# Performance work log

Measured on AMD Instinct MI355X. Metric: run time of the kernel, lower is better.

Reference implementation:

```python
import jax, jax.numpy as jnp
import numpy as np

EMBED = 1024
HEADS = 16
HEAD_DIM = EMBED // HEADS
B, S = 2, 2048


def setup_inputs() -> dict:
    key = jax.random.key(0)
    ks = jax.random.split(key, 9)
    std = 1.0 / np.sqrt(EMBED)
    def lin(k):
        kw, kb = jax.random.split(k)
        W = jax.random.uniform(kw, (EMBED, EMBED), jnp.float32, -std, std)
        b = jax.random.uniform(kb, (EMBED,), jnp.float32, -std, std)
        return W, b
    Wq, bq = lin(ks[0])
    Wk, bk = lin(ks[1])
    Wv, bv = lin(ks[2])
    Wo, bo = lin(ks[3])
    x = jax.random.normal(ks[4], (B, S, EMBED), jnp.float32)
    return {"x": x, "Wq": Wq, "bq": bq, "Wk": Wk, "bk": bk,
            "Wv": Wv, "bv": bv, "Wo": Wo, "bo": bo}


def reference(x, Wq, bq, Wk, bk, Wv, bv, Wo, bo):
    b, s, e = x.shape
    # projections (torch Linear: x @ W^T + b; here W stored as [in,out])
    Q = x @ Wq + bq
    K = x @ Wk + bk
    V = x @ Wv + bv
    # [b, h, s, d]
    Q = Q.reshape(b, s, HEADS, HEAD_DIM).transpose(0, 2, 1, 3)
    K = K.reshape(b, s, HEADS, HEAD_DIM).transpose(0, 2, 1, 3)
    V = V.reshape(b, s, HEADS, HEAD_DIM).transpose(0, 2, 1, 3)
    scores = jnp.einsum('bhqd,bhkd->bhqk', Q, K) / np.sqrt(HEAD_DIM)
    # causal mask: positions k > q masked to -inf
    causal = jnp.tril(jnp.ones((s, s), dtype=bool))
    scores = jnp.where(causal[None, None], scores, -jnp.inf)
    weights = jax.nn.softmax(scores, axis=-1)
    out = jnp.einsum('bhqk,bhkd->bhqd', weights, V)
    out = out.transpose(0, 2, 1, 3).reshape(b, s, e)
    return out @ Wo + bo
```

## Files before the change

### kernel.cpp

```cpp
#include <hip/hip_runtime.h>
#include <hip/hip_bf16.h>
#include <stdint.h>

#define EMBED 1024
#define HEADS 16
#define HDIM 64
#define BATCH 2
#define SEQ 2048
#define NROWS (BATCH*SEQ)

typedef __attribute__((ext_vector_type(8))) short short8;
typedef __attribute__((ext_vector_type(4))) float f32x4;

#define LOG2E 1.44269504088896f

__device__ __forceinline__ unsigned short f2bf(float f) {
    __hip_bfloat16 b = __float2bfloat16(f);
    return *reinterpret_cast<unsigned short*>(&b);
}

__device__ __forceinline__ unsigned cvt_pk_bf16(float lo, float hi) {
    unsigned r;
    asm("v_cvt_pk_bf16_f32 %0, %1, %2" : "=v"(r) : "v"(lo), "v"(hi));
    return r;
}

__device__ __forceinline__ short8 mk8(unsigned a, unsigned b, unsigned c, unsigned d) {
    union { unsigned u[4]; short8 s; } x;
    x.u[0] = a; x.u[1] = b; x.u[2] = c; x.u[3] = d;
    return x.s;
}

__device__ __forceinline__ void g2l16(const void* g, void* l) {
    __builtin_amdgcn_global_load_lds(
        (const __attribute__((address_space(1))) unsigned int*)g,
        (__attribute__((address_space(3))) unsigned int*)l, 16, 0, 0);
}

__global__ void prep_kernel(const float* __restrict__ x,
                            unsigned short* __restrict__ xb,
                            const float* __restrict__ W0,
                            const float* __restrict__ W1,
                            const float* __restrict__ W2,
                            const float* __restrict__ W3,
                            unsigned short* __restrict__ dst) {
    __shared__ float tile[32][33];
    const int id = blockIdx.x;
    const int t = threadIdx.x;
    if (id < 4096) {
        const int z = id >> 10;
        const int by = (id >> 5) & 31;
        const int bx = id & 31;
        const float* W = (z == 0) ? W0 : (z == 1) ? W1 : (z == 2) ? W2 : W3;
        unsigned short* Wt = dst + (size_t)z * EMBED * EMBED;
        const int tx = t & 31, ty = t >> 5;
#pragma unroll
        for (int r = 0; r < 4; r++) {
            int i = by * 32 + ty + r * 8;
            int o = bx * 32 + tx;
            tile[ty + r * 8][tx] = W[(size_t)i * EMBED + o];
        }
        __syncthreads();
        int i2 = by * 32 + tx;
#pragma unroll
        for (int r = 0; r < 4; r++) {
            int o2 = bx * 32 + ty + r * 8;
            Wt[(size_t)o2 * EMBED + i2] = f2bf(tile[tx][ty + r * 8]);
        }
    } else {
        int i = (id - 4096) * 256 + t;
        float4 v = reinterpret_cast<const float4*>(x)[i];
        ushort4 o;
        o.x = f2bf(v.x); o.y = f2bf(v.y); o.z = f2bf(v.z); o.w = f2bf(v.w);
        reinterpret_cast<ushort4*>(xb)[i] = o;
    }
}

template<int MODE, int BM, int BN, int PIPE>
__global__ __launch_bounds__(256)
void gemm_kernel(const unsigned short* __restrict__ A,
                 const unsigned short* __restrict__ B,
                 int K,
                 unsigned short* __restrict__ Qo,
                 unsigned short* __restrict__ Ko,
                 unsigned short* __restrict__ Vto,
                 const float* __restrict__ bq,
                 const float* __restrict__ bk,
                 const float* __restrict__ bvv,
                 float* __restrict__ Co,
                 const float* __restrict__ bo) {
    constexpr int AI = BM / 32;
    constexpr int BJ = BN / 32;
    constexpr int NBUF = PIPE ? 2 : 1;
    __shared__ __attribute__((aligned(16))) unsigned short As[NBUF][BM * 64];
    __shared__ __attribute__((aligned(16))) unsigned short Bs[NBUF][BN * 64];
    const int t = threadIdx.x;
    const int lane = t & 63;
    const int w = t >> 6;
    const int wr = w >> 1, wc = w & 1;
    const int l15 = lane & 15, l16 = lane >> 4;

    int bx, by;
    {
        const int xcd = blockIdx.x & 7;
        const int r = blockIdx.x >> 3;
        if (MODE == 0) {
            bx = (xcd & 1) * 12 + r % 12;
            by = (xcd >> 1) * 8 + r / 12;
        } else {
            bx = r & 15;
            by = xcd * 8 + (r >> 4);
        }
    }
    const int m0 = by * BM;
    const int n0 = bx * BN;

    f32x4 acc[AI][BJ];
#pragma unroll
    for (int i = 0; i < AI; i++)
#pragma unroll
        for (int j = 0; j < BJ; j++) acc[i][j] = (f32x4){0.f, 0.f, 0.f, 0.f};

    auto stage = [&](int k0, int buf) {
#pragma unroll
        for (int i = 0; i < BM / 32; i++) {
            int c = i * 256 + t;
            int row = c >> 3;
            int lc = (c & 7) ^ (row & 7);
            g2l16(A + (size_t)(m0 + row) * K + k0 + lc * 8,
                  As[buf] + (size_t)(i * 256 + (t & ~63)) * 8);
        }
#pragma unroll
        for (int i = 0; i < BN / 32; i++) {
            int c = i * 256 + t;
            int row = c >> 3;
            int lc = (c & 7) ^ (row & 7);
            g2l16(B + (size_t)(n0 + row) * K + k0 + lc * 8,
                  Bs[buf] + (size_t)(i * 256 + (t & ~63)) * 8);
        }
    };

    auto compute = [&](int buf) {
#pragma unroll
        for (int kk = 0; kk < 2; kk++) {
            short8 a[AI], b[BJ];
#pragma unroll
            for (int ai = 0; ai < AI; ai++) {
                int row = wr * (BM / 2) + ai * 16 + l15;
                int ch = kk * 4 + l16;
                a[ai] = *reinterpret_cast<const short8*>(
                    As[buf] + row * 64 + ((ch ^ (row & 7)) << 3));
            }
#pragma unroll
            for (int bj = 0; bj < BJ; bj++) {
                int row = wc * (BN / 2) + bj * 16 + l15;
                int ch = kk * 4 + l16;
                b[bj] = *reinterpret_cast<const short8*>(
                    Bs[buf] + row * 64 + ((ch ^ (row & 7)) << 3));
            }
            __builtin_amdgcn_s_setprio(1);
#pragma unroll
            for (int ai = 0; ai < AI; ai++)
#pragma unroll
                for (int bj = 0; bj < BJ; bj++)
                    acc[ai][bj] = __builtin_amdgcn_mfma_f32_16x16x32_bf16(
                        a[ai], b[bj], acc[ai][bj], 0, 0, 0);
            __builtin_amdgcn_s_setprio(0);
        }
    };

    if (PIPE) {
        const int ntk = K >> 6;
        stage(0, 0);
        asm volatile("s_waitcnt vmcnt(0)" ::: "memory");
        __builtin_amdgcn_s_barrier();
        asm volatile("" ::: "memory");
        for (int tk = 0; tk < ntk; tk++) {
            if (tk + 1 < ntk) stage((tk + 1) << 6, (tk + 1) & 1);
            compute(tk & 1);
            asm volatile("s_waitcnt vmcnt(0)" ::: "memory");
            __builtin_amdgcn_s_barrier();
            asm volatile("" ::: "memory");
        }
    } else {
        for (int k0 = 0; k0 < K; k0 += 64) {
            __syncthreads();
            stage(k0, 0);
            __syncthreads();
            compute(0);
        }
    }

    if (MODE == 0) {
        const int which = n0 >> 10;
        const int coln = n0 & 1023;
        const float* bias = which == 0 ? bq : (which == 1 ? bk : bvv);
        const float scale = which == 0 ? 0.125f * LOG2E : 1.0f;
#pragma unroll
        for (int ai = 0; ai < AI; ai++) {
            int rowb = m0 + wr * (BM / 2) + ai * 16 + l16 * 4;
            int b_ = rowb >> 11;
            int s = rowb & 2047;
#pragma unroll
            for (int bj = 0; bj < BJ; bj++) {
                int col = coln + wc * (BN / 2) + bj * 16 + l15;
                float bsv = bias[col];
                int h = col >> 6, d = col & 63;
                if (which < 2) {
                    unsigned short* dst = (which == 0) ? Qo : Ko;
                    size_t base = ((size_t)(b_ * HEADS + h)) * SEQ * HDIM;
#pragma unroll
                    for (int r = 0; r < 4; r++) {
                        float v = (acc[ai][bj][r] + bsv) * scale;
                        dst[base + (size_t)(s + r) * HDIM + d] = f2bf(v);
                    }
                } else {
                    ushort4 pk;
                    pk.x = f2bf(acc[ai][bj][0] + bsv);
                    pk.y = f2bf(acc[ai][bj][1] + bsv);
                    pk.z = f2bf(acc[ai][bj][2] + bsv);
                    pk.w = f2bf(acc[ai][bj][3] + bsv);
                    int cs = (s >> 2) & 15;
                    int ps = (cs & 8) | ((cs & 3) << 1) | ((cs >> 2) & 1);
                    size_t off = ((size_t)(b_ * HEADS + h) * HDIM + d) * SEQ +
                                 (size_t)((s & ~63) | (ps << 2));
                    *reinterpret_cast<ushort4*>(Vto + off) = pk;
                }
            }
        }
    } else {
#pragma unroll
        for (int ai = 0; ai < AI; ai++) {
            int rowb = m0 + wr * (BM / 2) + ai * 16 + l16 * 4;
#pragma unroll
            for (int bj = 0; bj < BJ; bj++) {
                int col = n0 + wc * (BN / 2) + bj * 16 + l15;
                float bsv = bo[col];
#pragma unroll
                for (int r = 0; r < 4; r++)
                    Co[(size_t)(rowb + r) * EMBED + col] = acc[ai][bj][r] + bsv;
            }
        }
    }
}

__device__ __forceinline__ void stage_kv(const unsigned short* __restrict__ Kg,
                                         const unsigned short* __restrict__ Vg,
                                         int kv0, unsigned short* Ksb,
                                         unsigned short* Vsb, int tl) {
#pragma unroll
    for (int i = 0; i < 4; i++) {
        int c = i * 128 + tl;
        int row = c >> 3;
        int lc = (c & 7) ^ (row & 7);
        g2l16(Kg + (size_t)(kv0 + row) * HDIM + lc * 8,
              Ksb + (i * 128 + (tl & ~63)) * 8);
    }
#pragma unroll
    for (int i = 0; i < 4; i++) {
        int c = i * 128 + tl;
        int d = c >> 3;
        int lc = (c & 7) ^ (d & 7);
        g2l16(Vg + (size_t)d * SEQ + kv0 + lc * 8,
              Vsb + (i * 128 + (tl & ~63)) * 8);
    }
}

__global__ __launch_bounds__(256, 2)
void attn_kernel(const unsigned short* __restrict__ Q,
                 const unsigned short* __restrict__ Kk,
                 const unsigned short* __restrict__ Vt,
                 unsigned short* __restrict__ O) {
    __shared__ __attribute__((aligned(16))) unsigned short Ks[4][64 * 64];
    __shared__ __attribute__((aligned(16))) unsigned short Vs[4][64 * 64];

    const int t = threadIdx.x;
    const int lane = t & 63;
    const int w = t >> 6;
    const int wq = w >> 1;
    const int wk = w & 1;
    const int l15 = lane & 15, l16 = lane >> 4;

    const int id = blockIdx.x;
    const int xcd = id & 7;
    const int u = id >> 3;
    const int bh = xcd * 4 + (u & 3);
    const int su = u >> 2;
    const int qi = (su < 16) ? su : 47 - su;
    const int q0 = qi * 64;
    const size_t base = (size_t)bh * SEQ * HDIM;
    const unsigned short* Kg = Kk + base;
    const unsigned short* Vg = Vt + base;
    const int qrow0 = q0 + wq * 32;

    short8 qf[2][2];
    {
        const unsigned short* Qg = Q + base + (size_t)qrow0 * HDIM;
#pragma unroll
        for (int qb = 0; qb < 2; qb++)
#pragma unroll
            for (int kc = 0; kc < 2; kc++)
                qf[qb][kc] = *reinterpret_cast<const short8*>(
                    Qg + (qb * 16 + l15) * HDIM + (kc * 4 + l16) * 8);
    }

    f32x4 oacc[2][4];
#pragma unroll
    for (int qb = 0; qb < 2; qb++)
#pragma unroll
        for (int nd = 0; nd < 4; nd++) oacc[qb][nd] = (f32x4){0.f, 0.f, 0.f, 0.f};
    float m_run[2] = {-1e30f, -1e30f};
    float l_run[2] = {0.f, 0.f};

    const int nt = qi + 1;
    const int nsuper = (nt + 1) >> 1;

    auto stagepair = [&](int ta, int tb) {
        if (t < 128) {
            if (ta < nt) stage_kv(Kg, Vg, ta * 64, Ks[ta & 3], Vs[ta & 3], t);
        } else {
            if (tb < nt) stage_kv(Kg, Vg, tb * 64, Ks[tb & 3], Vs[tb & 3], t - 128);
        }
    };

    auto qkt = [&](f32x4 (&sc)[2][4], const unsigned short* Kb) {
#pragma unroll
        for (int qb = 0; qb < 2; qb++)
#pragma unroll
            for (int kb = 0; kb < 4; kb++) sc[qb][kb] = (f32x4){0.f, 0.f, 0.f, 0.f};
#pragma unroll
        for (int kc = 0; kc < 2; kc++) {
            short8 ka[4];
#pragma unroll
            for (int kb = 0; kb < 4; kb++) {
                int row = kb * 16 + l15;
                ka[kb] = *reinterpret_cast<const short8*>(
                    Kb + row * 64 + (((kc * 4 + l16) ^ (row & 7)) << 3));
            }
            __builtin_amdgcn_s_setprio(1);
#pragma unroll
            for (int qb = 0; qb < 2; qb++)
#pragma unroll
                for (int kb = 0; kb < 4; kb++)
                    sc[qb][kb] = __builtin_amdgcn_mfma_f32_16x16x32_bf16(
                        ka[kb], qf[qb][kc], sc[qb][kb], 0, 0, 0);
            __builtin_amdgcn_s_setprio(0);
        }
    };

    auto softmax_pv = [&](f32x4 (&sc)[2][4], const unsigned short* Vb, bool diag) {
        if (diag) {
#pragma unroll
            for (int qb = 0; qb < 2; qb++) {
                const int qloc = wq * 32 + qb * 16 + l15;
#pragma unroll
                for (int kb = 0; kb < 4; kb++)
#pragma unroll
                    for (int r = 0; r < 4; r++) {
                        int kloc = kb * 16 + l16 * 4 + r;
                        sc[qb][kb][r] = (kloc > qloc) ? -1e30f : sc[qb][kb][r];
                    }
            }
        }
        float vmax[2];
        bool need = false;
#pragma unroll
        for (int qb = 0; qb < 2; qb++) {
            float mx = -1e30f;
#pragma unroll
            for (int kb = 0; kb < 4; kb++)
                mx = fmaxf(mx, fmaxf(fmaxf(sc[qb][kb][0], sc[qb][kb][1]),
                                     fmaxf(sc[qb][kb][2], sc[qb][kb][3])));
            vmax[qb] = mx;
            need = need || (mx > m_run[qb] + 8.0f);
        }
        if (__any(need)) {
#pragma unroll
            for (int qb = 0; qb < 2; qb++) {
                float mx = vmax[qb];
                mx = fmaxf(mx, __shfl_xor(mx, 16));
                mx = fmaxf(mx, __shfl_xor(mx, 32));
                float mn = fmaxf(m_run[qb], mx);
                float sf = __builtin_amdgcn_exp2f(m_run[qb] - mn);
                m_run[qb] = mn;
                l_run[qb] *= sf;
#pragma unroll
                for (int r = 0; r < 4; r++) {
                    float sfr = __shfl(sf, l16 * 4 + r);
#pragma unroll
                    for (int nd = 0; nd < 4; nd++) oacc[qb][nd][r] *= sfr;
                }
            }
        }
        short8 pa[2][2];
#pragma unroll
        for (int qb = 0; qb < 2; qb++) {
            float p[4][4];
            float ps = 0.f;
#pragma unroll
            for (int kb = 0; kb < 4; kb++)
#pragma unroll
                for (int r = 0; r < 4; r++) {
                    p[kb][r] = __builtin_amdgcn_exp2f(sc[qb][kb][r] - m_run[qb]);
                    ps += p[kb][r];
                }
            pa[qb][0] = mk8(cvt_pk_bf16(p[0][0], p[0][1]),
                            cvt_pk_bf16(p[0][2], p[0][3]),
                            cvt_pk_bf16(p[1][0], p[1][1]),
                            cvt_pk_bf16(p[1][2], p[1][3]));
            pa[qb][1] = mk8(cvt_pk_bf16(p[2][0], p[2][1]),
                            cvt_pk_bf16(p[2][2], p[2][3]),
                            cvt_pk_bf16(p[3][0], p[3][1]),
                            cvt_pk_bf16(p[3][2], p[3][3]));
            l_run[qb] += ps;
        }
#pragma unroll
        for (int m = 0; m < 2; m++) {
            short8 vb[4];
#pragma unroll
            for (int nd = 0; nd < 4; nd++) {
                int row = nd * 16 + l15;
                vb[nd] = *reinterpret_cast<const short8*>(
                    Vb + row * 64 + (((m * 4 + l16) ^ (row & 7)) << 3));
            }
            __builtin_amdgcn_s_setprio(1);
#pragma unroll
            for (int qb = 0; qb < 2; qb++)
#pragma unroll
                for (int nd = 0; nd < 4; nd++)
                    oacc[qb][nd] = __builtin_amdgcn_mfma_f32_16x16x32_bf16(
                        pa[qb][m], vb[nd], oacc[qb][nd], 0, 0, 0);
            __builtin_amdgcn_s_setprio(0);
        }
    };

    f32x4 sc[2][4];

    stagepair(0, 1);
    asm volatile("s_waitcnt vmcnt(0)" ::: "memory");
    __builtin_amdgcn_s_barrier();
    asm volatile("" ::: "memory");
    stagepair(2, 3);
    int myt = wk;
    if (myt < nt) qkt(sc, Ks[myt & 3]);

    for (int j = 1; j < nsuper; j++) {
        if (myt < nt) softmax_pv(sc, Vs[myt & 3], false);
        asm volatile("s_waitcnt vmcnt(0)" ::: "memory");
        __builtin_amdgcn_s_barrier();
        asm volatile("" ::: "memory");
        stagepair(2 * j + 2, 2 * j + 3);
        int tc = 2 * j + wk;
        if (tc < nt) qkt(sc, Ks[tc & 3]);
        myt = tc;
    }
    if (myt < nt) softmax_pv(sc, Vs[myt & 3], myt == nt - 1);

    __syncthreads();
    float* po = reinterpret_cast<float*>(&Ks[0][0]);
    float* pml = reinterpret_cast<float*>(&Vs[0][0]);
    if (wk == 1) {
#pragma unroll
        for (int qb = 0; qb < 2; qb++) {
#pragma unroll
            for (int nd = 0; nd < 4; nd++)
                reinterpret_cast<f32x4*>(po)[(((wq << 1) | qb) * 4 + nd) * 64 + lane] =
                    oacc[qb][nd];
            pml[((((wq << 1) | qb) * 64) + lane) * 2]     = m_run[qb];
            pml[((((wq << 1) | qb) * 64) + lane) * 2 + 1] = l_run[qb];
        }
    }
    __syncthreads();
    if (wk == 0) {
        const int b_ = bh >> 4, h = bh & 15;
#pragma unroll
        for (int qb = 0; qb < 2; qb++) {
            float m1 = pml[((((wq << 1) | qb) * 64) + lane) * 2];
            float l1 = pml[((((wq << 1) | qb) * 64) + lane) * 2 + 1];
            float ms = fmaxf(m_run[qb], m1);
            float a0 = __builtin_amdgcn_exp2f(m_run[qb] - ms);
            float a1 = __builtin_amdgcn_exp2f(m1 - ms);
            float lmp = l_run[qb] * a0 + l1 * a1;
            lmp += __shfl_xor(lmp, 16);
            lmp += __shfl_xor(lmp, 32);
            f32x4 o1[4];
#pragma unroll
            for (int nd = 0; nd < 4; nd++)
                o1[nd] = reinterpret_cast<f32x4*>(po)[(((wq << 1) | qb) * 4 + nd) * 64 + lane];
            float li = 1.0f / lmp;
#pragma unroll
            for (int r = 0; r < 4; r++) {
                float a0r = __shfl(a0, l16 * 4 + r);
                float a1r = __shfl(a1, l16 * 4 + r);
                float lir = __shfl(li, l16 * 4 + r);
                int row = b_ * SEQ + qrow0 + qb * 16 + l16 * 4 + r;
#pragma unroll
                for (int nd = 0; nd < 4; nd++) {
                    float v = oacc[qb][nd][r] * a0r + o1[nd][r] * a1r;
                    O[(size_t)row * EMBED + h * 64 + nd * 16 + l15] = f2bf(v * lir);
                }
            }
        }
    }
}

extern "C" void kernel_launch(void* const* d_in, const int* in_sizes, int n_in,
                              void* d_out, int out_size, void* d_ws, size_t ws_size,
                              hipStream_t stream) {
    (void)in_sizes; (void)n_in; (void)out_size; (void)ws_size;
    const float* x  = (const float*)d_in[0];
    const float* Wq = (const float*)d_in[1];
    const float* bq = (const float*)d_in[2];
    const float* Wk = (const float*)d_in[3];
    const float* bk = (const float*)d_in[4];
    const float* Wv = (const float*)d_in[5];
    const float* bv = (const float*)d_in[6];
    const float* Wo = (const float*)d_in[7];
    const float* bo = (const float*)d_in[8];
    float* out = (float*)d_out;

    unsigned short* xb   = (unsigned short*)d_ws;
    unsigned short* Wqkv = xb + (size_t)NROWS * EMBED;
    unsigned short* Wot  = Wqkv + (size_t)3 * EMBED * EMBED;
    unsigned short* Qb   = Wot + (size_t)EMBED * EMBED;
    unsigned short* Kb   = Qb + (size_t)NROWS * EMBED;
    unsigned short* Vtb  = Kb + (size_t)NROWS * EMBED;
    unsigned short* attn = Vtb + (size_t)NROWS * EMBED;

    prep_kernel<<<8192, 256, 0, stream>>>(x, xb, Wq, Wk, Wv, Wo, Wqkv);

    gemm_kernel<0, 128, 128, 0><<<768, 256, 0, stream>>>(
        xb, Wqkv, EMBED, Qb, Kb, Vtb, bq, bk, bv, nullptr, nullptr);

    attn_kernel<<<1024, 256, 0, stream>>>(Qb, Kb, Vtb, attn);

    gemm_kernel<1, 64, 64, 1><<<1024, 256, 0, stream>>>(
        attn, Wot, EMBED, nullptr, nullptr, nullptr, nullptr, nullptr, nullptr,
        out, bo);
}
```

Baseline: 91.07 us.

## Restructure attention to 128-row Q tiles with four query waves, no KV split

The attention kernel now gives each block 128 query rows, one 32-row slice per wave, and drops the two-way split of KV tiles across waves along with the shared-memory merge of partial softmax state. KV staging becomes a simple double buffer loaded by all 256 threads. LDS drops from 4 to 2 buffers and launch bounds rise to 4 blocks per CU, with half as many blocks. The aim is to reuse each K/V tile across more query rows and remove the merge step, at the cost of less work per KV tile per wave, a barrier every tile, and waves sitting idle on tiles past their causal limit.

```diff
diff --git a/kernel.cpp b/kernel.cpp
--- a/kernel.cpp
+++ b/kernel.cpp
@@ -247,38 +247,36 @@
 __device__ __forceinline__ void stage_kv(const unsigned short* __restrict__ Kg,
                                          const unsigned short* __restrict__ Vg,
                                          int kv0, unsigned short* Ksb,
-                                         unsigned short* Vsb, int tl) {
-#pragma unroll
-    for (int i = 0; i < 4; i++) {
-        int c = i * 128 + tl;
+                                         unsigned short* Vsb, int t) {
+#pragma unroll
+    for (int i = 0; i < 2; i++) {
+        int c = i * 256 + t;
         int row = c >> 3;
         int lc = (c & 7) ^ (row & 7);
         g2l16(Kg + (size_t)(kv0 + row) * HDIM + lc * 8,
-              Ksb + (i * 128 + (tl & ~63)) * 8);
-    }
-#pragma unroll
-    for (int i = 0; i < 4; i++) {
-        int c = i * 128 + tl;
+              Ksb + (i * 256 + (t & ~63)) * 8);
+    }
+#pragma unroll
+    for (int i = 0; i < 2; i++) {
+        int c = i * 256 + t;
         int d = c >> 3;
         int lc = (c & 7) ^ (d & 7);
         g2l16(Vg + (size_t)d * SEQ + kv0 + lc * 8,
-              Vsb + (i * 128 + (tl & ~63)) * 8);
-    }
-}
-
-__global__ __launch_bounds__(256, 2)
+              Vsb + (i * 256 + (t & ~63)) * 8);
+    }
+}
+
+__global__ __launch_bounds__(256, 4)
 void attn_kernel(const unsigned short* __restrict__ Q,
                  const unsigned short* __restrict__ Kk,
                  const unsigned short* __restrict__ Vt,
                  unsigned short* __restrict__ O) {
-    __shared__ __attribute__((aligned(16))) unsigned short Ks[4][64 * 64];
-    __shared__ __attribute__((aligned(16))) unsigned short Vs[4][64 * 64];
+    __shared__ __attribute__((aligned(16))) unsigned short Ks[2][64 * 64];
+    __shared__ __attribute__((aligned(16))) unsigned short Vs[2][64 * 64];
 
     const int t = threadIdx.x;
     const int lane = t & 63;
     const int w = t >> 6;
-    const int wq = w >> 1;
-    const int wk = w & 1;
     const int l15 = lane & 15, l16 = lane >> 4;
 
     const int id = blockIdx.x;
@@ -286,12 +284,12 @@
     const int u = id >> 3;
     const int bh = xcd * 4 + (u & 3);
     const int su = u >> 2;
-    const int qi = (su < 16) ? su : 47 - su;
-    const int q0 = qi * 64;
+    const int qi = (su < 8) ? su : 23 - su;
+    const int q0 = qi * 128;
     const size_t base = (size_t)bh * SEQ * HDIM;
     const unsigned short* Kg = Kk + base;
     const unsigned short* Vg = Vt + base;
-    const int qrow0 = q0 + wq * 32;
+    const int qrow0 = q0 + w * 32;
 
     short8 qf[2][2];
     {
@@ -312,16 +310,7 @@
     float m_run[2] = {-1e30f, -1e30f};
     float l_run[2] = {0.f, 0.f};
 
-    const int nt = qi + 1;
-    const int nsuper = (nt + 1) >> 1;
-
-    auto stagepair = [&](int ta, int tb) {
-        if (t < 128) {
-            if (ta < nt) stage_kv(Kg, Vg, ta * 64, Ks[ta & 3], Vs[ta & 3], t);
-        } else {
-            if (tb < nt) stage_kv(Kg, Vg, tb * 64, Ks[tb & 3], Vs[tb & 3], t - 128);
-        }
-    };
+    const int nt = 2 * qi + 2;
 
     auto qkt = [&](f32x4 (&sc)[2][4], const unsigned short* Kb) {
 #pragma unroll
@@ -348,17 +337,17 @@
         }
     };
 
-    auto softmax_pv = [&](f32x4 (&sc)[2][4], const unsigned short* Vb, bool diag) {
-        if (diag) {
+    auto softmax_pv = [&](f32x4 (&sc)[2][4], const unsigned short* Vb, int kv0) {
+        if (kv0 + 63 > qrow0) {
 #pragma unroll
             for (int qb = 0; qb < 2; qb++) {
-                const int qloc = wq * 32 + qb * 16 + l15;
+                const int qg = qrow0 + qb * 16 + l15;
 #pragma unroll
                 for (int kb = 0; kb < 4; kb++)
 #pragma unroll
                     for (int r = 0; r < 4; r++) {
-                        int kloc = kb * 16 + l16 * 4 + r;
-                        sc[qb][kb][r] = (kloc > qloc) ? -1e30f : sc[qb][kb][r];
+                        int kg = kv0 + kb * 16 + l16 * 4 + r;
+                        sc[qb][kb][r] = (kg > qg) ? -1e30f : sc[qb][kb][r];
                     }
             }
         }
@@ -436,70 +425,35 @@
 
     f32x4 sc[2][4];
 
-    stagepair(0, 1);
-    asm volatile("s_waitcnt vmcnt(0)" ::: "memory");
-    __builtin_amdgcn_s_barrier();
-    asm volatile("" ::: "memory");
-    stagepair(2, 3);
-    int myt = wk;
-    if (myt < nt) qkt(sc, Ks[myt & 3]);
-
-    for (int j = 1; j < nsuper; j++) {
-        if (myt < nt) softmax_pv(sc, Vs[myt & 3], false);
+    stage_kv(Kg, Vg, 0, Ks[0], Vs[0], t);
+    for (int tk = 0; tk < nt; tk++) {
         asm volatile("s_waitcnt vmcnt(0)" ::: "memory");
         __builtin_amdgcn_s_barrier();
         asm volatile("" ::: "memory");
-        stagepair(2 * j + 2, 2 * j + 3);
-        int tc = 2 * j + wk;
-        if (tc < nt) qkt(sc, Ks[tc & 3]);
-        myt = tc;
-    }
-    if (myt < nt) softmax_pv(sc, Vs[myt & 3], myt == nt - 1);
-
-    __syncthreads();
-    float* po = reinterpret_cast<float*>(&Ks[0][0]);
-    float* pml = reinterpret_cast<float*>(&Vs[0][0]);
-    if (wk == 1) {
-#pragma unroll
-        for (int qb = 0; qb < 2; qb++) {
+        if (tk + 1 < nt)
+            stage_kv(Kg, Vg, (tk + 1) * 64, Ks[(tk + 1) & 1], Vs[(tk + 1) & 1], t);
+        const int kv0 = tk * 64;
+        if (kv0 <= qrow0 + 31) {
+            qkt(sc, Ks[tk & 1]);
+            softmax_pv(sc, Vs[tk & 1], kv0);
+        }
+    }
+
+    const int b_ = bh >> 4, h = bh & 15;
+#pragma unroll
+    for (int qb = 0; qb < 2; qb++) {
+        float lmp = l_run[qb];
+        lmp += __shfl_xor(lmp, 16);
+        lmp += __shfl_xor(lmp, 32);
+        float li = 1.0f / lmp;
+#pragma unroll
+        for (int r = 0; r < 4; r++) {
+            float lir = __shfl(li, l16 * 4 + r);
+            int row = b_ * SEQ + qrow0 + qb * 16 + l16 * 4 + r;
 #pragma unroll
             for (int nd = 0; nd < 4; nd++)
-                reinterpret_cast<f32x4*>(po)[(((wq << 1) | qb) * 4 + nd) * 64 + lane] =
-                    oacc[qb][nd];
-            pml[((((wq << 1) | qb) * 64) + lane) * 2]     = m_run[qb];
-            pml[((((wq << 1) | qb) * 64) + lane) * 2 + 1] = l_run[qb];
-        }
-    }
-    __syncthreads();
-    if (wk == 0) {
-        const int b_ = bh >> 4, h = bh & 15;
-#pragma unroll
-        for (int qb = 0; qb < 2; qb++) {
-            float m1 = pml[((((wq << 1) | qb) * 64) + lane) * 2];
-            float l1 = pml[((((wq << 1) | qb) * 64) + lane) * 2 + 1];
-            float ms = fmaxf(m_run[qb], m1);
-            float a0 = __builtin_amdgcn_exp2f(m_run[qb] - ms);
-            float a1 = __builtin_amdgcn_exp2f(m1 - ms);
-            float lmp = l_run[qb] * a0 + l1 * a1;
-            lmp += __shfl_xor(lmp, 16);
-            lmp += __shfl_xor(lmp, 32);
-            f32x4 o1[4];
-#pragma unroll
-            for (int nd = 0; nd < 4; nd++)
-                o1[nd] = reinterpret_cast<f32x4*>(po)[(((wq << 1) | qb) * 4 + nd) * 64 + lane];
-            float li = 1.0f / lmp;
-#pragma unroll
-            for (int r = 0; r < 4; r++) {
-                float a0r = __shfl(a0, l16 * 4 + r);
-                float a1r = __shfl(a1, l16 * 4 + r);
-                float lir = __shfl(li, l16 * 4 + r);
-                int row = b_ * SEQ + qrow0 + qb * 16 + l16 * 4 + r;
-#pragma unroll
-                for (int nd = 0; nd < 4; nd++) {
-                    float v = oacc[qb][nd][r] * a0r + o1[nd][r] * a1r;
-                    O[(size_t)row * EMBED + h * 64 + nd * 16 + l15] = f2bf(v * lir);
-                }
-            }
+                O[(size_t)row * EMBED + h * 64 + nd * 16 + l15] =
+                    f2bf(oacc[qb][nd][r] * lir);
         }
     }
 }
@@ -532,7 +486,7 @@
     gemm_kernel<0, 128, 128, 0><<<768, 256, 0, stream>>>(
         xb, Wqkv, EMBED, Qb, Kb, Vtb, bq, bk, bv, nullptr, nullptr);
 
-    attn_kernel<<<1024, 256, 0, stream>>>(Qb, Kb, Vtb, attn);
+    attn_kernel<<<512, 256, 0, stream>>>(Qb, Kb, Vtb, attn);
 
     gemm_kernel<1, 64, 64, 1><<<1024, 256, 0, stream>>>(
         attn, Wot, EMBED, nullptr, nullptr, nullptr, nullptr, nullptr, nullptr,
```

Measured after the change: 116.5 us. +27.9%, slower.

## Enlarge attention query tile to 128 rows with 8 waves sharing KV tiles

Applied to the files above, without the earlier changes.

Each attention block now handles 128 query rows with 512 threads instead of 64 rows with 256, so every staged K/V tile in shared memory is reused by twice as many waves. The grid halves, staging is split across 256 threads per half, and the causal mask moves to global indices. Waves skip KV tiles that lie entirely above their rows. The trade-off is fewer, larger blocks and more within-block imbalance on diagonal tiles, which may hurt occupancy and load balance.

```diff
diff --git a/kernel.cpp b/kernel.cpp
--- a/kernel.cpp
+++ b/kernel.cpp
@@ -249,24 +249,24 @@
                                          int kv0, unsigned short* Ksb,
                                          unsigned short* Vsb, int tl) {
 #pragma unroll
-    for (int i = 0; i < 4; i++) {
-        int c = i * 128 + tl;
+    for (int i = 0; i < 2; i++) {
+        int c = i * 256 + tl;
         int row = c >> 3;
         int lc = (c & 7) ^ (row & 7);
         g2l16(Kg + (size_t)(kv0 + row) * HDIM + lc * 8,
-              Ksb + (i * 128 + (tl & ~63)) * 8);
-    }
-#pragma unroll
-    for (int i = 0; i < 4; i++) {
-        int c = i * 128 + tl;
+              Ksb + (i * 256 + (tl & ~63)) * 8);
+    }
+#pragma unroll
+    for (int i = 0; i < 2; i++) {
+        int c = i * 256 + tl;
         int d = c >> 3;
         int lc = (c & 7) ^ (d & 7);
         g2l16(Vg + (size_t)d * SEQ + kv0 + lc * 8,
-              Vsb + (i * 128 + (tl & ~63)) * 8);
-    }
-}
-
-__global__ __launch_bounds__(256, 2)
+              Vsb + (i * 256 + (tl & ~63)) * 8);
+    }
+}
+
+__global__ __launch_bounds__(512, 2)
 void attn_kernel(const unsigned short* __restrict__ Q,
                  const unsigned short* __restrict__ Kk,
                  const unsigned short* __restrict__ Vt,
@@ -286,8 +286,8 @@
     const int u = id >> 3;
     const int bh = xcd * 4 + (u & 3);
     const int su = u >> 2;
-    const int qi = (su < 16) ? su : 47 - su;
-    const int q0 = qi * 64;
+    const int qi = (su < 8) ? su : 23 - su;
+    const int q0 = qi * 128;
     const size_t base = (size_t)bh * SEQ * HDIM;
     const unsigned short* Kg = Kk + base;
     const unsigned short* Vg = Vt + base;
@@ -312,14 +312,14 @@
     float m_run[2] = {-1e30f, -1e30f};
     float l_run[2] = {0.f, 0.f};
 
-    const int nt = qi + 1;
-    const int nsuper = (nt + 1) >> 1;
+    const int nt = 2 * qi + 2;
+    const int nsuper = nt >> 1;
 
     auto stagepair = [&](int ta, int tb) {
-        if (t < 128) {
+        if (t < 256) {
             if (ta < nt) stage_kv(Kg, Vg, ta * 64, Ks[ta & 3], Vs[ta & 3], t);
         } else {
-            if (tb < nt) stage_kv(Kg, Vg, tb * 64, Ks[tb & 3], Vs[tb & 3], t - 128);
+            if (tb < nt) stage_kv(Kg, Vg, tb * 64, Ks[tb & 3], Vs[tb & 3], t - 256);
         }
     };
 
@@ -348,17 +348,17 @@
         }
     };
 
-    auto softmax_pv = [&](f32x4 (&sc)[2][4], const unsigned short* Vb, bool diag) {
-        if (diag) {
+    auto softmax_pv = [&](f32x4 (&sc)[2][4], const unsigned short* Vb, int kv0) {
+        if (kv0 + 63 > qrow0) {
 #pragma unroll
             for (int qb = 0; qb < 2; qb++) {
-                const int qloc = wq * 32 + qb * 16 + l15;
+                const int qg = qrow0 + qb * 16 + l15;
 #pragma unroll
                 for (int kb = 0; kb < 4; kb++)
 #pragma unroll
                     for (int r = 0; r < 4; r++) {
-                        int kloc = kb * 16 + l16 * 4 + r;
-                        sc[qb][kb][r] = (kloc > qloc) ? -1e30f : sc[qb][kb][r];
+                        int kg = kv0 + kb * 16 + l16 * 4 + r;
+                        sc[qb][kb][r] = (kg > qg) ? -1e30f : sc[qb][kb][r];
                     }
             }
         }
@@ -442,19 +442,22 @@
     asm volatile("" ::: "memory");
     stagepair(2, 3);
     int myt = wk;
-    if (myt < nt) qkt(sc, Ks[myt & 3]);
+    bool act = (myt < nt) && (myt * 64 <= qrow0 + 31);
+    if (act) qkt(sc, Ks[myt & 3]);
 
     for (int j = 1; j < nsuper; j++) {
-        if (myt < nt) softmax_pv(sc, Vs[myt & 3], false);
+        if (act) softmax_pv(sc, Vs[myt & 3], myt * 64);
         asm volatile("s_waitcnt vmcnt(0)" ::: "memory");
         __builtin_amdgcn_s_barrier();
         asm volatile("" ::: "memory");
         stagepair(2 * j + 2, 2 * j + 3);
         int tc = 2 * j + wk;
-        if (tc < nt) qkt(sc, Ks[tc & 3]);
+        bool act2 = (tc < nt) && (tc * 64 <= qrow0 + 31);
+        if (act2) qkt(sc, Ks[tc & 3]);
         myt = tc;
-    }
-    if (myt < nt) softmax_pv(sc, Vs[myt & 3], myt == nt - 1);
+        act = act2;
+    }
+    if (act) softmax_pv(sc, Vs[myt & 3], myt * 64);
 
     __syncthreads();
     float* po = reinterpret_cast<float*>(&Ks[0][0]);
@@ -462,12 +465,13 @@
     if (wk == 1) {
 #pragma unroll
         for (int qb = 0; qb < 2; qb++) {
+            int g = (wq << 1) | qb;
 #pragma unroll
             for (int nd = 0; nd < 4; nd++)
-                reinterpret_cast<f32x4*>(po)[(((wq << 1) | qb) * 4 + nd) * 64 + lane] =
+                reinterpret_cast<f32x4*>(po)[(g * 4 + nd) * 64 + lane] =
                     oacc[qb][nd];
-            pml[((((wq << 1) | qb) * 64) + lane) * 2]     = m_run[qb];
-            pml[((((wq << 1) | qb) * 64) + lane) * 2 + 1] = l_run[qb];
+            pml[(g * 64 + lane) * 2]     = m_run[qb];
+            pml[(g * 64 + lane) * 2 + 1] = l_run[qb];
         }
     }
     __syncthreads();
@@ -475,8 +479,9 @@
         const int b_ = bh >> 4, h = bh & 15;
 #pragma unroll
         for (int qb = 0; qb < 2; qb++) {
-            float m1 = pml[((((wq << 1) | qb) * 64) + lane) * 2];
-            float l1 = pml[((((wq << 1) | qb) * 64) + lane) * 2 + 1];
+            int g = (wq << 1) | qb;
+            float m1 = pml[(g * 64 + lane) * 2];
+            float l1 = pml[(g * 64 + lane) * 2 + 1];
             float ms = fmaxf(m_run[qb], m1);
             float a0 = __builtin_amdgcn_exp2f(m_run[qb] - ms);
             float a1 = __builtin_amdgcn_exp2f(m1 - ms);
@@ -486,7 +491,7 @@
             f32x4 o1[4];
 #pragma unroll
             for (int nd = 0; nd < 4; nd++)
-                o1[nd] = reinterpret_cast<f32x4*>(po)[(((wq << 1) | qb) * 4 + nd) * 64 + lane];
+                o1[nd] = reinterpret_cast<f32x4*>(po)[(g * 4 + nd) * 64 + lane];
             float li = 1.0f / lmp;
 #pragma unroll
             for (int r = 0; r < 4; r++) {
@@ -532,7 +537,7 @@
     gemm_kernel<0, 128, 128, 0><<<768, 256, 0, stream>>>(
         xb, Wqkv, EMBED, Qb, Kb, Vtb, bq, bk, bv, nullptr, nullptr);
 
-    attn_kernel<<<1024, 256, 0, stream>>>(Qb, Kb, Vtb, attn);
+    attn_kernel<<<512, 512, 0, stream>>>(Qb, Kb, Vtb, attn);
 
     gemm_kernel<1, 64, 64, 1><<<1024, 256, 0, stream>>>(
         attn, Wot, EMBED, nullptr, nullptr, nullptr, nullptr, nullptr, nullptr,
```

Result: slower. 93.76 us (+2.9%).
